# Performance work log

Measured on AMD Instinct MI355X. Metric: run time of the kernel, lower is better.

The kernel has to match this reference:

```python
import jax, jax.numpy as jnp
import numpy as np

N_SU = 8
DATA_DIM = N_SU * N_SU - 1  # 63
BATCH = 1048576


def _gell_mann(n):
    """Generalized Gell-Mann matrices of su(n), Tr(L_a L_b) = 2 delta_ab."""
    mats = []
    for j in range(n):
        for k in range(j + 1, n):
            m = np.zeros((n, n), dtype=np.complex128); m[j, k] = 1.0; m[k, j] = 1.0
            mats.append(m)
            m = np.zeros((n, n), dtype=np.complex128); m[j, k] = -1.0j; m[k, j] = 1.0j
            mats.append(m)
    for l in range(1, n):
        m = np.zeros((n, n), dtype=np.complex128)
        c = np.sqrt(2.0 / (l * (l + 1)))
        for j in range(l):
            m[j, j] = c
        m[l, l] = -l * c
        mats.append(m)
    return np.stack(mats)


def _structure_const(n):
    """f_abc = Tr([L_a,L_b]L_c)/(4i), d_abc = Tr({L_a,L_b}L_c)/4 (both real)."""
    L = _gell_mann(n)                                  # (D, n, n)
    P = np.einsum('aij,bjk->abik', L, L)               # L_a L_b
    comm = P - P.transpose(1, 0, 2, 3)
    anti = P + P.transpose(1, 0, 2, 3)
    f = (np.einsum('abik,cki->abc', comm, L) / 4.0j).real
    d = (np.einsum('abik,cki->abc', anti, L) / 4.0).real
    return f.astype(np.float32), d.astype(np.float32)

F_CONST, D_CONST = _structure_const(N_SU)              # (D, D, D) each, compile-time constants
TRI = np.stack(np.triu_indices(DATA_DIM, 0))           # incl. diagonal
TRI1 = np.stack(np.triu_indices(DATA_DIM, 1))          # strict upper


def setup_inputs() -> dict:
    key = jax.random.key(0)
    k1, k2, k3, k4, k5 = jax.random.split(key, 5)
    D = DATA_DIM
    return {
        'x': jax.random.normal(k1, (BATCH, D), dtype=jnp.float32),
        'r_x': jax.random.uniform(k2, (D * (D + 1) // 2,), dtype=jnp.float32),
        'r_y': jax.random.uniform(k3, (D * (D - 1) // 2,), dtype=jnp.float32),
        'N': jax.random.uniform(k4, (1,), dtype=jnp.float32),
        'omega': jax.random.uniform(k5, (D,), dtype=jnp.float32),
    }


def _forward(x, r_x, r_y, N, omega):
    f = jnp.asarray(F_CONST)
    d = jnp.asarray(D_CONST)
    D = DATA_DIM
    # NOTE: faithful to the torch source, where `v_x = v_y = torch.zeros(...)`
    # aliases ONE tensor: r_y overwrites r_x on the strict upper triangle and
    # v_x is v_y, which makes c_im exactly zero.
    v = jnp.zeros((D, D), dtype=x.dtype)
    v = v.at[TRI[0], TRI[1]].set(r_x)
    v = v.at[TRI1[0], TRI1[1]].set(r_y)
    v_x = v
    v_y = v
    c_re = v_x.T @ v_x + v_y.T @ v_y                   # einsum('ki,kj->ij', v, v) x2
    c_re = c_re / jnp.trace(c_re)
    c_im = v_x.T @ v_y - v_y.T @ v_x                   # exactly zero (aliasing)
    c_re = N * c_re

    # Precompute the small (D,D) superoperator coefficient matrices once, then
    # apply them to the batch with plain matmuls (bn,mn->bm).
    A1 = jnp.einsum('mjk,ij->mik', f, c_re)
    M_re1 = jnp.einsum('mik,nik->mn', A1, f)           # 'mjk,nik,ij->mn'
    A2 = jnp.einsum('mik,ij->mjk', f, c_re)
    M_re2 = jnp.einsum('mjk,njk->mn', A2, f)           # 'mik,njk,ij->mn'
    B1 = jnp.einsum('mjk,ij->mik', f, c_im)
    M_im1 = jnp.einsum('mik,nik->mn', B1, d)
    B2 = jnp.einsum('mik,ij->mjk', f, c_im)
    M_im2 = jnp.einsum('mjk,njk->mn', B2, d)
    M = -2.0 * M_re1 - 2.0 * M_re2 - 2.0 * M_im1 + 2.0 * M_im2

    d_super_x = x @ M.T                                 # (B, D)
    H = 8.0 * jnp.einsum('kij,k->ij', f, omega)
    h_commutator_x = x @ H.T                            # 'kij,k,bj->bi'
    tr_id = -8.0 * jnp.einsum('imj,ij->m', f, c_im)     # (D,), zero here

    S_x = h_commutator_x + d_super_x
    T_x = x + tr_id
    L_x = S_x + T_x
    return x + 0.01 * L_x


def reference(x, r_x, r_y, N, omega):
    return _forward(x, r_x, r_y, N, omega)
```

## Files before the change

kernel.cpp:

```cpp
#include <hip/hip_runtime.h>
#include <hip/hip_bf16.h>

#define DD 63
#define DD2 (DD * DD)
#define NSU 8

typedef __attribute__((ext_vector_type(8))) short short8;
typedef __attribute__((ext_vector_type(4))) float f32x4;

__device__ float  g_F[DD2 * DD];
__device__ float  g_B[DD * DD2];
__device__ float  g_cc[DD2];
__device__ unsigned short g_Gb[64 * 64];

__device__ __forceinline__ unsigned short f2bf(float f) {
    union { float f; unsigned u; } v; v.f = f;
    unsigned r = v.u + 0x7FFFu + ((v.u >> 16) & 1u);
    return (unsigned short)(r >> 16);
}

__device__ __forceinline__ void fill_L(int a, float (*re)[NSU], float (*im)[NSU]) {
    if (a < 56) {
        int p = a >> 1;
        int j = 0, rem = p;
        while (rem >= 7 - j) { rem -= 7 - j; ++j; }
        int k = j + 1 + rem;
        if ((a & 1) == 0) { re[j][k] = 1.f; re[k][j] = 1.f; }
        else             { im[j][k] = -1.f; im[k][j] = 1.f; }
    } else {
        int l = a - 55;
        float c = sqrtf(2.f / (float)(l * (l + 1)));
        for (int j = 0; j < l; ++j) re[j][j] = c;
        re[l][l] = -(float)l * c;
    }
}

__global__ __launch_bounds__(64) void setup1_kernel(const float* __restrict__ r_x,
                                                    const float* __restrict__ r_y) {
    const int t = threadIdx.x;
    if (blockIdx.x < DD2) {
        __shared__ float Ar[NSU][NSU], Ai[NSU][NSU], Br[NSU][NSU], Bi[NSU][NSU];
        __shared__ float Cr[NSU][NSU], Ci[NSU][NSU];
        const int a = blockIdx.x / DD, b = blockIdx.x % DD;
        const int r = t >> 3, c = t & 7;
        Ar[r][c] = 0.f; Ai[r][c] = 0.f; Br[r][c] = 0.f; Bi[r][c] = 0.f;
        __syncthreads();
        if (t == 0) fill_L(a, Ar, Ai);
        if (t == 1) fill_L(b, Br, Bi);
        __syncthreads();
        float pr = 0.f, pi = 0.f, qr = 0.f, qi = 0.f;
        #pragma unroll
        for (int k = 0; k < NSU; ++k) {
            pr += Ar[r][k] * Br[k][c] - Ai[r][k] * Bi[k][c];
            pi += Ar[r][k] * Bi[k][c] + Ai[r][k] * Br[k][c];
            qr += Br[r][k] * Ar[k][c] - Bi[r][k] * Ai[k][c];
            qi += Br[r][k] * Ai[k][c] + Bi[r][k] * Ar[k][c];
        }
        Cr[r][c] = pr - qr;
        Ci[r][c] = pi - qi;
        __syncthreads();
        if (t < DD) {
            float im;
            if (t < 56) {
                int p = t >> 1;
                int j = 0, rem = p;
                while (rem >= 7 - j) { rem -= 7 - j; ++j; }
                int k = j + 1 + rem;
                if ((t & 1) == 0) im = Ci[j][k] + Ci[k][j];
                else              im = Cr[j][k] - Cr[k][j];
            } else {
                int l = t - 55;
                float cd = sqrtf(2.f / (float)(l * (l + 1)));
                float s = 0.f;
                for (int j = 0; j < l; ++j) s += Ci[j][j];
                im = cd * s - (float)l * cd * Ci[l][l];
            }
            g_F[(a * DD + b) * DD + t] = 0.25f * im;
        }
    } else {
        __shared__ float v[DD2];
        const int jcol = blockIdx.x - DD2;
        for (int idx = t; idx < DD2; idx += 64) {
            int i = idx / DD, j = idx - i * DD;
            float val = 0.f;
            if (j > i)       val = r_y[62 * i - (i * (i - 1)) / 2 + (j - i - 1)];
            else if (j == i) val = r_x[63 * i - (i * (i - 1)) / 2];
            v[idx] = val;
        }
        __syncthreads();
        if (t < DD) {
            float s = 0.f;
            for (int k = 0; k < DD; ++k) s = fmaf(v[k * DD + t], v[k * DD + jcol], s);
            g_cc[t * DD + jcol] = s;
        }
    }
}

__global__ __launch_bounds__(256) void buildB_kernel() {
    __shared__ float scc[DD2];
    __shared__ float sf[DD2];
    const int t = threadIdx.x;
    const int n = blockIdx.x;
    for (int idx = t; idx < DD2; idx += 256) {
        scc[idx] = g_cc[idx];
        sf[idx]  = g_F[n * DD2 + idx];
    }
    __syncthreads();
    for (int idx = t; idx < DD2; idx += 256) {
        const int j = idx / DD, k = idx % DD;
        float s = 0.f;
        for (int i = 0; i < DD; ++i) s = fmaf(scc[i * DD + j], sf[i * DD + k], s);
        g_B[n * DD2 + idx] = s;
    }
}

__global__ __launch_bounds__(64) void buildKt_kernel(const float* __restrict__ omega,
                                                     const float* __restrict__ Np) {
    const int m = blockIdx.x >> 6;
    const int n = blockIdx.x & 63;
    const int lane = threadIdx.x;
    if (m >= DD || n >= DD) {
        if (lane == 0) g_Gb[m * 64 + n] = 0;
        return;
    }
    float d = (lane < DD) ? g_cc[lane * 64] : 0.f;
    #pragma unroll
    for (int off = 32; off > 0; off >>= 1) d += __shfl_xor(d, off);
    const float scale = Np[0] / d;

    const float* __restrict__ Fm = g_F + m * DD2;
    const float* __restrict__ Bn = g_B + n * DD2;
    float p = 0.f;
    for (int idx = lane; idx < DD2; idx += 64) p = fmaf(Fm[idx], Bn[idx], p);
    float h = (lane < DD) ? g_F[lane * DD2 + m * DD + n] * omega[lane] : 0.f;
    #pragma unroll
    for (int off = 32; off > 0; off >>= 1) {
        p += __shfl_down(p, off);
        h += __shfl_down(h, off);
    }
    if (lane == 0)
        g_Gb[m * 64 + n] = f2bf(0.01f * (-4.f * scale * p + 8.f * h)
                                + ((m == n) ? 1.01f : 0.f));
}

__global__ __launch_bounds__(256) void apply_kernel(const float* __restrict__ x,
                                                    float* __restrict__ out,
                                                    int ntiles, int nwaves) {
    __shared__ float slab[4][16 * 64];
    const int t = threadIdx.x;
    const int w = t >> 6, lane = t & 63;
    const int mrow = lane & 15, q = lane >> 4;
    float* __restrict__ S = slab[w];

    const short8* __restrict__ gG = (const short8*)g_Gb;
    short8 bfrag[2][4];
    #pragma unroll
    for (int kt = 0; kt < 2; ++kt)
        #pragma unroll
        for (int nt = 0; nt < 4; ++nt)
            bfrag[kt][nt] = gG[(nt * 16 + mrow) * 8 + kt * 4 + q];

    if (lane < 16) S[lane * 64 + (((15 ^ lane) << 2) | 3)] = 0.f;

    int soff[4][4];
    #pragma unroll
    for (int i = 0; i < 4; ++i) {
        const int f = i * 64 + lane;
        #pragma unroll
        for (int j = 0; j < 4; ++j) {
            const int e = 4 * f + j;
            const int r = e / 63, c = e - r * 63;
            soff[i][j] = r * 64 + ((((c >> 2) ^ r) << 2) | (c & 3));
        }
    }
    const bool act3 = (lane < 60);

    int tile = blockIdx.x * 4 + w;
    if (tile >= ntiles) return;

    float4 ld[4];
    {
        const float4* __restrict__ gp = (const float4*)(x + (size_t)tile * (16 * DD));
        ld[0] = gp[lane]; ld[1] = gp[lane + 64]; ld[2] = gp[lane + 128];
        if (act3) ld[3] = gp[lane + 192];
    }

    while (true) {
        #pragma unroll
        for (int i = 0; i < 3; ++i) {
            S[soff[i][0]] = ld[i].x; S[soff[i][1]] = ld[i].y;
            S[soff[i][2]] = ld[i].z; S[soff[i][3]] = ld[i].w;
        }
        if (act3) {
            S[soff[3][0]] = ld[3].x; S[soff[3][1]] = ld[3].y;
            S[soff[3][2]] = ld[3].z; S[soff[3][3]] = ld[3].w;
        }
        const size_t tb = (size_t)tile * (16 * DD);
        const int next = tile + nwaves;

        float va[2][8];
        #pragma unroll
        for (int kt = 0; kt < 2; ++kt) {
            const int c0 = 8 * kt + 2 * q;
            *(float4*)&va[kt][0] = *(const float4*)&S[mrow * 64 + (((c0    ) ^ mrow) << 2)];
            *(float4*)&va[kt][4] = *(const float4*)&S[mrow * 64 + (((c0 + 1) ^ mrow) << 2)];
        }

        if (next < ntiles) {
            const float4* __restrict__ gp = (const float4*)(x + (size_t)next * (16 * DD));
            ld[0] = gp[lane]; ld[1] = gp[lane + 64]; ld[2] = gp[lane + 128];
            if (act3) ld[3] = gp[lane + 192];
        }

        short8 af[2];
        #pragma unroll
        for (int kt = 0; kt < 2; ++kt)
            #pragma unroll
            for (int j = 0; j < 8; ++j) {
                __hip_bfloat16 h = __float2bfloat16(va[kt][j]);
                af[kt][j] = *reinterpret_cast<short*>(&h);
            }

        f32x4 acc[4] = {{0.f,0.f,0.f,0.f},{0.f,0.f,0.f,0.f},
                        {0.f,0.f,0.f,0.f},{0.f,0.f,0.f,0.f}};
        #pragma unroll
        for (int nt = 0; nt < 4; ++nt) {
            acc[nt] = __builtin_amdgcn_mfma_f32_16x16x32_bf16(af[0], bfrag[0][nt], acc[nt], 0, 0, 0);
            acc[nt] = __builtin_amdgcn_mfma_f32_16x16x32_bf16(af[1], bfrag[1][nt], acc[nt], 0, 0, 0);
        }

        #pragma unroll
        for (int nt = 0; nt < 4; ++nt) {
            const int ocol = nt * 16 + mrow;
            if (ocol < DD) {
                #pragma unroll
                for (int r = 0; r < 4; ++r) {
                    const int orow = q * 4 + r;
                    S[orow * 64 + ((((ocol >> 2) ^ orow) << 2) | (ocol & 3))] = acc[nt][r];
                }
            }
        }

        #pragma unroll
        for (int i = 0; i < 3; ++i) {
            float4 o;
            o.x = S[soff[i][0]]; o.y = S[soff[i][1]];
            o.z = S[soff[i][2]]; o.w = S[soff[i][3]];
            ((float4*)(out + tb))[i * 64 + lane] = o;
        }
        if (act3) {
            float4 o;
            o.x = S[soff[3][0]]; o.y = S[soff[3][1]];
            o.z = S[soff[3][2]]; o.w = S[soff[3][3]];
            ((float4*)(out + tb))[192 + lane] = o;
        }

        if (next >= ntiles) break;
        tile = next;
    }
}

extern "C" void kernel_launch(void* const* d_in, const int* in_sizes, int n_in,
                              void* d_out, int out_size, void* d_ws, size_t ws_size,
                              hipStream_t stream) {
    const float* x     = (const float*)d_in[0];
    const float* r_x   = (const float*)d_in[1];
    const float* r_y   = (const float*)d_in[2];
    const float* Np    = (const float*)d_in[3];
    const float* omega = (const float*)d_in[4];
    float* out = (float*)d_out;

    const int rows = in_sizes[0] / DD;
    const int ntiles = rows / 16;
    const int ablocks = 2048;
    const int nwaves = ablocks * 4;

    setup1_kernel<<<DD2 + DD, 64, 0, stream>>>(r_x, r_y);
    buildB_kernel<<<DD, 256, 0, stream>>>();
    buildKt_kernel<<<64 * 64, 64, 0, stream>>>(omega, Np);
    apply_kernel<<<ablocks, 256, 0, stream>>>(x, out, ntiles, nwaves);
}
```

Measured before the change: 184.0 us.

## Fuse setup and apply kernels into one cooperative kernel with grid syncs

Merges the three setup kernels and the batched apply kernel into a single cooperative launch of 1024 blocks, separated by grid-wide barriers, and falls back to the old four-launch path if the cooperative launch fails. The goal is to remove inter-kernel launch gaps and run the small setup stages across more waves at once. In exchange the apply phase gets half as many blocks (1024 instead of 2048), pays for three grid syncs, and requires every block to be co-resident.

```diff
diff --git a/kernel.cpp b/kernel.cpp
--- a/kernel.cpp
+++ b/kernel.cpp
@@ -1,9 +1,14 @@
 #include <hip/hip_runtime.h>
 #include <hip/hip_bf16.h>
+#include <hip/hip_cooperative_groups.h>
+
+namespace cg = cooperative_groups;
 
 #define DD 63
 #define DD2 (DD * DD)
 #define NSU 8
+#define NBLK 1024
+#define NWAVE (NBLK * 4)
 
 typedef __attribute__((ext_vector_type(8))) short short8;
 typedef __attribute__((ext_vector_type(4))) float f32x4;
@@ -19,19 +24,264 @@
     return (unsigned short)(r >> 16);
 }
 
-__device__ __forceinline__ void fill_L(int a, float (*re)[NSU], float (*im)[NSU]) {
+__device__ __forceinline__ void fill_L(int a, float* re, float* im) {
     if (a < 56) {
         int p = a >> 1;
         int j = 0, rem = p;
         while (rem >= 7 - j) { rem -= 7 - j; ++j; }
         int k = j + 1 + rem;
-        if ((a & 1) == 0) { re[j][k] = 1.f; re[k][j] = 1.f; }
-        else             { im[j][k] = -1.f; im[k][j] = 1.f; }
+        if ((a & 1) == 0) { re[j * 8 + k] = 1.f; re[k * 8 + j] = 1.f; }
+        else             { im[j * 8 + k] = -1.f; im[k * 8 + j] = 1.f; }
     } else {
         int l = a - 55;
         float c = sqrtf(2.f / (float)(l * (l + 1)));
-        for (int j = 0; j < l; ++j) re[j][j] = c;
-        re[l][l] = -(float)l * c;
+        for (int j = 0; j < l; ++j) re[j * 9] = c;
+        re[l * 9] = -(float)l * c;
+    }
+}
+
+__global__ __launch_bounds__(256, 4)
+void fused_kernel(const float* __restrict__ x, const float* __restrict__ r_x,
+                  const float* __restrict__ r_y, const float* __restrict__ Np,
+                  const float* __restrict__ omega, float* __restrict__ out,
+                  int ntiles) {
+    __shared__ __align__(16) unsigned char smem[16384];
+    const int t = threadIdx.x;
+    const int bid = blockIdx.x;
+    const int w = t >> 6, lane = t & 63;
+
+    if (bid < 1008) {
+        const int u = bid * 4 + w;
+        if (u < DD2) {
+            float* M = (float*)(smem + (w << 12));
+            float *Ar = M, *Ai = M + 64, *Br = M + 128, *Bi = M + 192;
+            float *Cr = M + 256, *Ci = M + 320;
+            const int a = u / DD, b = u % DD;
+            const int r = lane >> 3, c = lane & 7;
+            Ar[lane] = 0.f; Ai[lane] = 0.f; Br[lane] = 0.f; Bi[lane] = 0.f;
+            if (lane == 0) fill_L(a, Ar, Ai);
+            if (lane == 1) fill_L(b, Br, Bi);
+            float pr = 0.f, pi = 0.f, qr = 0.f, qi = 0.f;
+            #pragma unroll
+            for (int k = 0; k < NSU; ++k) {
+                pr += Ar[r * 8 + k] * Br[k * 8 + c] - Ai[r * 8 + k] * Bi[k * 8 + c];
+                pi += Ar[r * 8 + k] * Bi[k * 8 + c] + Ai[r * 8 + k] * Br[k * 8 + c];
+                qr += Br[r * 8 + k] * Ar[k * 8 + c] - Bi[r * 8 + k] * Ai[k * 8 + c];
+                qi += Br[r * 8 + k] * Ai[k * 8 + c] + Bi[r * 8 + k] * Ar[k * 8 + c];
+            }
+            Cr[lane] = pr - qr;
+            Ci[lane] = pi - qi;
+            if (lane < DD) {
+                float im;
+                if (lane < 56) {
+                    int p = lane >> 1;
+                    int j = 0, rem = p;
+                    while (rem >= 7 - j) { rem -= 7 - j; ++j; }
+                    int k = j + 1 + rem;
+                    if ((lane & 1) == 0) im = Ci[j * 8 + k] + Ci[k * 8 + j];
+                    else                 im = Cr[j * 8 + k] - Cr[k * 8 + j];
+                } else {
+                    int l = lane - 55;
+                    float cd = sqrtf(2.f / (float)(l * (l + 1)));
+                    float s = 0.f;
+                    for (int j = 0; j < l; ++j) s += Ci[j * 9];
+                    im = cd * s - (float)l * cd * Ci[l * 9];
+                }
+                g_F[u * DD + lane] = 0.25f * im;
+            }
+        }
+    } else {
+        const int cb = bid - 1008;
+        float* v = (float*)smem;
+        for (int idx = t; idx < DD2; idx += 256) {
+            int i = idx / DD, j = idx - i * DD;
+            float val = 0.f;
+            if (j > i)       val = r_y[62 * i - (i * (i - 1)) / 2 + (j - i - 1)];
+            else if (j == i) val = r_x[63 * i - (i * (i - 1)) / 2];
+            v[idx] = val;
+        }
+        __syncthreads();
+        for (int e = t; e < 63 * 4; e += 256) {
+            const int i = e % 63;
+            const int jj = cb * 4 + e / 63;
+            if (jj < DD) {
+                float s0 = 0.f, s1 = 0.f, s2 = 0.f, s3 = 0.f;
+                int k = 0;
+                for (; k + 3 < DD; k += 4) {
+                    s0 = fmaf(v[(k    ) * DD + i], v[(k    ) * DD + jj], s0);
+                    s1 = fmaf(v[(k + 1) * DD + i], v[(k + 1) * DD + jj], s1);
+                    s2 = fmaf(v[(k + 2) * DD + i], v[(k + 2) * DD + jj], s2);
+                    s3 = fmaf(v[(k + 3) * DD + i], v[(k + 3) * DD + jj], s3);
+                }
+                for (; k < DD; ++k) s0 = fmaf(v[k * DD + i], v[k * DD + jj], s0);
+                g_cc[i * DD + jj] = (s0 + s1) + (s2 + s3);
+            }
+        }
+    }
+
+    cg::this_grid().sync();
+
+    if (bid < 1008) {
+        const int n = bid >> 4, sl = bid & 15;
+        float* sf = (float*)smem;
+        for (int idx = t; idx < DD2; idx += 256) sf[idx] = g_F[n * DD2 + idx];
+        __syncthreads();
+        const int lo = sl * 249;
+        const int hi = (lo + 249 < DD2) ? lo + 249 : DD2;
+        for (int idx = lo + t; idx < hi; idx += 256) {
+            const int j = idx / DD, k = idx - j * DD;
+            float s0 = 0.f, s1 = 0.f, s2 = 0.f, s3 = 0.f;
+            int i = 0;
+            for (; i + 3 < DD; i += 4) {
+                s0 = fmaf(g_cc[(i    ) * DD + j], sf[(i    ) * DD + k], s0);
+                s1 = fmaf(g_cc[(i + 1) * DD + j], sf[(i + 1) * DD + k], s1);
+                s2 = fmaf(g_cc[(i + 2) * DD + j], sf[(i + 2) * DD + k], s2);
+                s3 = fmaf(g_cc[(i + 3) * DD + j], sf[(i + 3) * DD + k], s3);
+            }
+            for (; i < DD; ++i) s0 = fmaf(g_cc[i * DD + j], sf[i * DD + k], s0);
+            g_B[n * DD2 + idx] = (s0 + s1) + (s2 + s3);
+        }
+    }
+
+    cg::this_grid().sync();
+
+    {
+        const int u = bid * 4 + w;
+        const int m = u >> 6, n = u & 63;
+        if (m >= DD || n >= DD) {
+            if (lane == 0) g_Gb[m * 64 + n] = 0;
+        } else {
+            float d = (lane < DD) ? g_cc[lane * 64] : 0.f;
+            #pragma unroll
+            for (int off = 32; off > 0; off >>= 1) d += __shfl_xor(d, off);
+            const float scale = Np[0] / d;
+
+            const float* __restrict__ Fm = g_F + m * DD2;
+            const float* __restrict__ Bn = g_B + n * DD2;
+            float p = 0.f;
+            for (int idx = lane; idx < DD2; idx += 64) p = fmaf(Fm[idx], Bn[idx], p);
+            float h = (lane < DD) ? g_F[lane * DD2 + m * DD + n] * omega[lane] : 0.f;
+            #pragma unroll
+            for (int off = 32; off > 0; off >>= 1) {
+                p += __shfl_down(p, off);
+                h += __shfl_down(h, off);
+            }
+            if (lane == 0)
+                g_Gb[m * 64 + n] = f2bf(0.01f * (-4.f * scale * p + 8.f * h)
+                                        + ((m == n) ? 1.01f : 0.f));
+        }
+    }
+
+    cg::this_grid().sync();
+
+    const int mrow = lane & 15, q = lane >> 4;
+    float* __restrict__ S = (float*)smem + (w << 10);
+
+    const short8* __restrict__ gG = (const short8*)g_Gb;
+    short8 bfrag[2][4];
+    #pragma unroll
+    for (int kt = 0; kt < 2; ++kt)
+        #pragma unroll
+        for (int nt = 0; nt < 4; ++nt)
+            bfrag[kt][nt] = gG[(nt * 16 + mrow) * 8 + kt * 4 + q];
+
+    if (lane < 16) S[lane * 64 + (((15 ^ lane) << 2) | 3)] = 0.f;
+
+    int soff[4][4];
+    #pragma unroll
+    for (int i = 0; i < 4; ++i) {
+        const int f = i * 64 + lane;
+        #pragma unroll
+        for (int j = 0; j < 4; ++j) {
+            const int e = 4 * f + j;
+            const int r = e / 63, c = e - r * 63;
+            soff[i][j] = r * 64 + ((((c >> 2) ^ r) << 2) | (c & 3));
+        }
+    }
+    const bool act3 = (lane < 60);
+
+    int tile = bid * 4 + w;
+    if (tile >= ntiles) return;
+
+    float4 ld[4];
+    {
+        const float4* __restrict__ gp = (const float4*)(x + (size_t)tile * (16 * DD));
+        ld[0] = gp[lane]; ld[1] = gp[lane + 64]; ld[2] = gp[lane + 128];
+        if (act3) ld[3] = gp[lane + 192];
+    }
+
+    while (true) {
+        #pragma unroll
+        for (int i = 0; i < 3; ++i) {
+            S[soff[i][0]] = ld[i].x; S[soff[i][1]] = ld[i].y;
+            S[soff[i][2]] = ld[i].z; S[soff[i][3]] = ld[i].w;
+        }
+        if (act3) {
+            S[soff[3][0]] = ld[3].x; S[soff[3][1]] = ld[3].y;
+            S[soff[3][2]] = ld[3].z; S[soff[3][3]] = ld[3].w;
+        }
+        const size_t tb = (size_t)tile * (16 * DD);
+        const int next = tile + NWAVE;
+
+        float va[2][8];
+        #pragma unroll
+        for (int kt = 0; kt < 2; ++kt) {
+            const int c0 = 8 * kt + 2 * q;
+            *(float4*)&va[kt][0] = *(const float4*)&S[mrow * 64 + (((c0    ) ^ mrow) << 2)];
+            *(float4*)&va[kt][4] = *(const float4*)&S[mrow * 64 + (((c0 + 1) ^ mrow) << 2)];
+        }
+
+        if (next < ntiles) {
+            const float4* __restrict__ gp = (const float4*)(x + (size_t)next * (16 * DD));
+            ld[0] = gp[lane]; ld[1] = gp[lane + 64]; ld[2] = gp[lane + 128];
+            if (act3) ld[3] = gp[lane + 192];
+        }
+
+        short8 af[2];
+        #pragma unroll
+        for (int kt = 0; kt < 2; ++kt)
+            #pragma unroll
+            for (int j = 0; j < 8; ++j) {
+                __hip_bfloat16 h = __float2bfloat16(va[kt][j]);
+                af[kt][j] = *reinterpret_cast<short*>(&h);
+            }
+
+        f32x4 acc[4] = {{0.f,0.f,0.f,0.f},{0.f,0.f,0.f,0.f},
+                        {0.f,0.f,0.f,0.f},{0.f,0.f,0.f,0.f}};
+        #pragma unroll
+        for (int nt = 0; nt < 4; ++nt) {
+            acc[nt] = __builtin_amdgcn_mfma_f32_16x16x32_bf16(af[0], bfrag[0][nt], acc[nt], 0, 0, 0);
+            acc[nt] = __builtin_amdgcn_mfma_f32_16x16x32_bf16(af[1], bfrag[1][nt], acc[nt], 0, 0, 0);
+        }
+
+        #pragma unroll
+        for (int nt = 0; nt < 4; ++nt) {
+            const int ocol = nt * 16 + mrow;
+            if (ocol < DD) {
+                #pragma unroll
+                for (int r = 0; r < 4; ++r) {
+                    const int orow = q * 4 + r;
+                    S[orow * 64 + ((((ocol >> 2) ^ orow) << 2) | (ocol & 3))] = acc[nt][r];
+                }
+            }
+        }
+
+        #pragma unroll
+        for (int i = 0; i < 3; ++i) {
+            float4 o;
+            o.x = S[soff[i][0]]; o.y = S[soff[i][1]];
+            o.z = S[soff[i][2]]; o.w = S[soff[i][3]];
+            ((float4*)(out + tb))[i * 64 + lane] = o;
+        }
+        if (act3) {
+            float4 o;
+            o.x = S[soff[3][0]]; o.y = S[soff[3][1]];
+            o.z = S[soff[3][2]]; o.w = S[soff[3][3]];
+            ((float4*)(out + tb))[192 + lane] = o;
+        }
+
+        if (next >= ntiles) break;
+        tile = next;
     }
 }
 
@@ -39,11 +289,10 @@
                                                     const float* __restrict__ r_y) {
     const int t = threadIdx.x;
     if (blockIdx.x < DD2) {
-        __shared__ float Ar[NSU][NSU], Ai[NSU][NSU], Br[NSU][NSU], Bi[NSU][NSU];
-        __shared__ float Cr[NSU][NSU], Ci[NSU][NSU];
+        __shared__ float Ar[64], Ai[64], Br[64], Bi[64], Cr[64], Ci[64];
         const int a = blockIdx.x / DD, b = blockIdx.x % DD;
         const int r = t >> 3, c = t & 7;
-        Ar[r][c] = 0.f; Ai[r][c] = 0.f; Br[r][c] = 0.f; Bi[r][c] = 0.f;
+        Ar[t] = 0.f; Ai[t] = 0.f; Br[t] = 0.f; Bi[t] = 0.f;
         __syncthreads();
         if (t == 0) fill_L(a, Ar, Ai);
         if (t == 1) fill_L(b, Br, Bi);
@@ -51,13 +300,13 @@
         float pr = 0.f, pi = 0.f, qr = 0.f, qi = 0.f;
         #pragma unroll
         for (int k = 0; k < NSU; ++k) {
-            pr += Ar[r][k] * Br[k][c] - Ai[r][k] * Bi[k][c];
-            pi += Ar[r][k] * Bi[k][c] + Ai[r][k] * Br[k][c];
-            qr += Br[r][k] * Ar[k][c] - Bi[r][k] * Ai[k][c];
-            qi += Br[r][k] * Ai[k][c] + Bi[r][k] * Ar[k][c];
-        }
-        Cr[r][c] = pr - qr;
-        Ci[r][c] = pi - qi;
+            pr += Ar[r * 8 + k] * Br[k * 8 + c] - Ai[r * 8 + k] * Bi[k * 8 + c];
+            pi += Ar[r * 8 + k] * Bi[k * 8 + c] + Ai[r * 8 + k] * Br[k * 8 + c];
+            qr += Br[r * 8 + k] * Ar[k * 8 + c] - Bi[r * 8 + k] * Ai[k * 8 + c];
+            qi += Br[r * 8 + k] * Ai[k * 8 + c] + Bi[r * 8 + k] * Ar[k * 8 + c];
+        }
+        Cr[t] = pr - qr;
+        Ci[t] = pi - qi;
         __syncthreads();
         if (t < DD) {
             float im;
@@ -66,14 +315,14 @@
                 int j = 0, rem = p;
                 while (rem >= 7 - j) { rem -= 7 - j; ++j; }
                 int k = j + 1 + rem;
-                if ((t & 1) == 0) im = Ci[j][k] + Ci[k][j];
-                else              im = Cr[j][k] - Cr[k][j];
+                if ((t & 1) == 0) im = Ci[j * 8 + k] + Ci[k * 8 + j];
+                else              im = Cr[j * 8 + k] - Cr[k * 8 + j];
             } else {
                 int l = t - 55;
                 float cd = sqrtf(2.f / (float)(l * (l + 1)));
                 float s = 0.f;
-                for (int j = 0; j < l; ++j) s += Ci[j][j];
-                im = cd * s - (float)l * cd * Ci[l][l];
+                for (int j = 0; j < l; ++j) s += Ci[j * 9];
+                im = cd * s - (float)l * cd * Ci[l * 9];
             }
             g_F[(a * DD + b) * DD + t] = 0.25f * im;
         }
@@ -270,13 +519,18 @@
     const float* omega = (const float*)d_in[4];
     float* out = (float*)d_out;
 
-    const int rows = in_sizes[0] / DD;
-    const int ntiles = rows / 16;
-    const int ablocks = 2048;
-    const int nwaves = ablocks * 4;
-
-    setup1_kernel<<<DD2 + DD, 64, 0, stream>>>(r_x, r_y);
-    buildB_kernel<<<DD, 256, 0, stream>>>();
-    buildKt_kernel<<<64 * 64, 64, 0, stream>>>(omega, Np);
-    apply_kernel<<<ablocks, 256, 0, stream>>>(x, out, ntiles, nwaves);
-}
+    int rows = in_sizes[0] / DD;
+    int ntiles = rows / 16;
+
+    void* args[] = { (void*)&x, (void*)&r_x, (void*)&r_y, (void*)&Np,
+                     (void*)&omega, (void*)&out, (void*)&ntiles };
+    hipError_t e = hipLaunchCooperativeKernel((const void*)fused_kernel,
+                                              dim3(NBLK), dim3(256), args, 0, stream);
+    if (e != hipSuccess) {
+        (void)hipGetLastError();
+        setup1_kernel<<<DD2 + DD, 64, 0, stream>>>(r_x, r_y);
+        buildB_kernel<<<DD, 256, 0, stream>>>();
+        buildKt_kernel<<<64 * 64, 64, 0, stream>>>(omega, Np);
+        apply_kernel<<<2048, 256, 0, stream>>>(x, out, ntiles, 8192);
+    }
+}
```

Result: slower. 469.6 us (+155.2%).
